# Kernel optimization log

Hardware: AMD Instinct MI355X
Metric: run time of the kernel (lower is better)

Reference implementation:

```python
import jax, jax.numpy as jnp
import numpy as np

N_NODES = 50000
N_EDGES = 800000
DIM = 128
N_GRAPHS = 512
LEVELS = [2, 2, 2]  # GCN layers per hierarchy level
N_LAYERS = sum(LEVELS)
EPS = 1e-5


def setup_inputs() -> dict:
    key = jax.random.key(0)
    ks = jax.random.split(key, 8)
    x = jax.random.normal(ks[0], (N_NODES, DIM), dtype=jnp.float32)
    edge_index = jax.random.randint(ks[1], (2, N_EDGES), 0, N_NODES, dtype=jnp.int64)
    batch = jnp.sort(jax.random.randint(ks[2], (N_NODES,), 0, N_GRAPHS, dtype=jnp.int64))
    # stacked per-layer GCN params (all layers are DIM->DIM since input_dim==hidden_dim)
    s = 1.0 / np.sqrt(DIM)
    W = jax.random.uniform(ks[3], (N_LAYERS, DIM, DIM), minval=-s, maxval=s, dtype=jnp.float32)
    b = jnp.zeros((N_LAYERS, DIM), dtype=jnp.float32)
    gamma = jnp.ones((N_LAYERS, DIM), dtype=jnp.float32)
    beta = jnp.zeros((N_LAYERS, DIM), dtype=jnp.float32)
    sf = 1.0 / np.sqrt(DIM * len(LEVELS))
    Wf = jax.random.uniform(ks[4], (DIM * len(LEVELS), DIM), minval=-sf, maxval=sf, dtype=jnp.float32)
    bf = jnp.zeros((DIM,), dtype=jnp.float32)
    return {"x": x, "edge_index": edge_index, "batch": batch,
            "W": W, "b": b, "gamma": gamma, "beta": beta, "Wf": Wf, "bf": bf}


def reference(x, edge_index, batch, W, b, gamma, beta, Wf, bf):
    N = x.shape[0]
    # GCNConv: add self-loops, symmetric normalization deg^-1/2 A_hat deg^-1/2
    loop = jnp.arange(N, dtype=edge_index.dtype)
    src = jnp.concatenate([edge_index[0], loop])
    dst = jnp.concatenate([edge_index[1], loop])
    deg = jax.ops.segment_sum(jnp.ones_like(dst, dtype=x.dtype), dst, num_segments=N)
    dinv = jnp.where(deg > 0, jax.lax.rsqrt(deg), 0.0)
    norm = dinv[src] * dinv[dst]  # (E+N,)

    def gcn(h, Wl, bl):
        h = h @ Wl                                   # (N, DIM)
        msg = h[src] * norm[:, None]                 # gather + scale, (E+N, DIM)
        return jax.ops.segment_sum(msg, dst, num_segments=N) + bl

    def batchnorm_relu(h, g, be):
        mu = jnp.mean(h, axis=0)
        var = jnp.mean(jnp.square(h - mu), axis=0)   # biased var (training-mode BN)
        return jax.nn.relu(g * (h - mu) * jax.lax.rsqrt(var + EPS) + be)

    counts = jax.ops.segment_sum(jnp.ones((N,), x.dtype), batch, num_segments=N_GRAPHS)
    counts = jnp.maximum(counts, 1.0)[:, None]

    reps = []
    h = x
    li = 0
    for num_layers in LEVELS:
        for _ in range(num_layers):
            h = batchnorm_relu(gcn(h, W[li], b[li]), gamma[li], beta[li])
            li += 1
        reps.append(jax.ops.segment_sum(h, batch, num_segments=N_GRAPHS) / counts)
    fused = jnp.concatenate(reps, axis=1)            # (G, 3*DIM)
    return jax.nn.relu(fused @ Wf + bf)              # dropout is identity at inference
```

## Files before the change

kernel.cpp:

```cpp
#include <hip/hip_runtime.h>
#include <hip/hip_fp16.h>


#define DIM 128
#define NGRAPH 512
#define EPSV 1e-5f


__global__ __launch_bounds__(256) void k_count(const int* __restrict__ ei, int* __restrict__ cnt, int E) {
  int e = blockIdx.x * 256 + threadIdx.x;
  if (e < E) atomicAdd(&cnt[ei[E + e]], 1);
}

__global__ __launch_bounds__(512) void k_blocksum(const int* __restrict__ cnt, int* __restrict__ partial, int N) {
  __shared__ int sd[512];
  int idx = blockIdx.x * 512 + threadIdx.x;
  int v = (idx < N) ? cnt[idx] : 0;
  sd[threadIdx.x] = v;
  __syncthreads();
  for (int ofs = 256; ofs > 0; ofs >>= 1) {
    if (threadIdx.x < ofs) sd[threadIdx.x] += sd[threadIdx.x + ofs];
    __syncthreads();
  }
  if (threadIdx.x == 0) partial[blockIdx.x] = sd[0];
}

__global__ __launch_bounds__(128) void k_scanpartials(int* __restrict__ partial, int nb) {
  __shared__ int sp[128];
  int t = threadIdx.x;
  int v = (t < nb) ? partial[t] : 0;
  sp[t] = v;
  __syncthreads();
  for (int ofs = 1; ofs < 128; ofs <<= 1) {
    int a = (t >= ofs) ? sp[t - ofs] : 0;
    __syncthreads();
    sp[t] += a;
    __syncthreads();
  }
  if (t < nb) partial[t] = sp[t] - v;
}

__global__ __launch_bounds__(512) void k_scan_write(const int* __restrict__ cnt, const int* __restrict__ partial,
                                                    int* __restrict__ rowptr, float* __restrict__ dinv, int N) {
  __shared__ int sd[512];
  int tid = threadIdx.x;
  int idx = blockIdx.x * 512 + tid;
  int v = (idx < N) ? cnt[idx] : 0;
  sd[tid] = v;
  __syncthreads();
  for (int ofs = 1; ofs < 512; ofs <<= 1) {
    int a = (tid >= ofs) ? sd[tid - ofs] : 0;
    __syncthreads();
    sd[tid] += a;
    __syncthreads();
  }
  if (idx < N) {
    int excl = partial[blockIdx.x] + sd[tid] - v;
    rowptr[idx] = excl;
    dinv[idx] = rsqrtf((float)(v + 1));
    if (idx == N - 1) rowptr[N] = excl + v;
  }
}

__global__ __launch_bounds__(256) void k_fill(const int* __restrict__ ei, const int* __restrict__ rowptr,
                                              int* __restrict__ cursor, unsigned short* __restrict__ cols, int E) {
  int e = blockIdx.x * 256 + threadIdx.x;
  if (e >= E) return;
  int s = ei[e];
  int d = ei[E + e];
  int pos = rowptr[d] + atomicAdd(&cursor[d], 1);
  cols[pos] = (unsigned short)s;
}

__global__ __launch_bounds__(256) void k_gstart(const int* __restrict__ batch, int* __restrict__ start, int N) {
  int i = blockIdx.x * 256 + threadIdx.x;
  if (i >= N) return;
  int bi = batch[i];
  int prev = (i == 0) ? -1 : batch[i - 1];
  for (int g = prev + 1; g <= bi; ++g) start[g] = i;
  if (i == N - 1) {
    for (int g = bi + 1; g <= NGRAPH; ++g) start[g] = N;
  }
}

__global__ __launch_bounds__(512) void k_invcnt(const int* __restrict__ start, float* __restrict__ invcnt) {
  int g = threadIdx.x;
  if (g < NGRAPH) {
    int c = start[g + 1] - start[g];
    invcnt[g] = 1.0f / (float)max(c, 1);
  }
}


__device__ inline void fma4(float4& ar, float a, const float4& wv) {
  ar.x = fmaf(a, wv.x, ar.x);
  ar.y = fmaf(a, wv.y, ar.y);
  ar.z = fmaf(a, wv.z, ar.z);
  ar.w = fmaf(a, wv.w, ar.w);
}

__global__ __launch_bounds__(256) void k_gemm(const float* __restrict__ A32,
                                              const unsigned int* __restrict__ A16,
                                              const float* __restrict__ Wl,
                                              const float* __restrict__ scsh,
                                              const float* __restrict__ dinv,
                                              unsigned int* __restrict__ T, float* __restrict__ stats, int N) {
  __shared__ float sH[64][DIM];
  int tid = threadIdx.x;
  size_t pstride = (size_t)(N + 1) * 16;
  if (blockIdx.x == 0) {
    stats[tid] = 0.f;
    if (tid < 64) {
      int p = tid >> 4, sl = tid & 15;
      T[(size_t)p * pstride + (size_t)N * 16 + sl] = 0u;
    }
  }
  int row0 = blockIdx.x * 64;
#pragma unroll
  for (int i = 0; i < 8; ++i) {
    int fi = tid + i * 256;
    int r = fi >> 5, c4 = fi & 31;
    int row = row0 + r;
    float4 v = make_float4(0.f, 0.f, 0.f, 0.f);
    if (scsh) {
      if (row < N) {
        uint2 u = ((const uint2*)(A16 + (size_t)row * 64))[c4];
        float2 lo = __half22float2(*(__half2*)&u.x);
        float2 hi = __half22float2(*(__half2*)&u.y);
        float4 sc = ((const float4*)scsh)[c4];
        float4 sh = ((const float4*)(scsh + DIM))[c4];
        v.x = fmaxf(fmaf(lo.x, sc.x, sh.x), 0.f);
        v.y = fmaxf(fmaf(lo.y, sc.y, sh.y), 0.f);
        v.z = fmaxf(fmaf(hi.x, sc.z, sh.z), 0.f);
        v.w = fmaxf(fmaf(hi.y, sc.w, sh.w), 0.f);
      }
    } else {
      if (row < N) v = ((const float4*)(A32 + (size_t)row * DIM))[c4];
    }
    ((float4*)&sH[r][0])[c4] = v;
  }
  __syncthreads();
  int ct = tid & 31, rt = tid >> 5;
  const float4* Wv = (const float4*)Wl;
  float4 acc[8];
#pragma unroll
  for (int r = 0; r < 8; ++r) acc[r] = make_float4(0.f, 0.f, 0.f, 0.f);
  for (int k4 = 0; k4 < 32; ++k4) {
    float4 wv0 = Wv[(4 * k4 + 0) * 32 + ct];
    float4 wv1 = Wv[(4 * k4 + 1) * 32 + ct];
    float4 wv2 = Wv[(4 * k4 + 2) * 32 + ct];
    float4 wv3 = Wv[(4 * k4 + 3) * 32 + ct];
#pragma unroll
    for (int r = 0; r < 8; ++r) {
      float4 av = *(const float4*)&sH[rt + 8 * r][4 * k4];
      fma4(acc[r], av.x, wv0);
      fma4(acc[r], av.y, wv1);
      fma4(acc[r], av.z, wv2);
      fma4(acc[r], av.w, wv3);
    }
  }
  int panel = ct >> 3;
  int psl = (ct & 7) * 2;
  unsigned int* Tp = T + (size_t)panel * pstride;
#pragma unroll
  for (int r = 0; r < 8; ++r) {
    int row = row0 + rt + 8 * r;
    if (row < N) {
      float dr = dinv[row];
      __half2 h0 = __floats2half2_rn(acc[r].x * dr, acc[r].y * dr);
      __half2 h1 = __floats2half2_rn(acc[r].z * dr, acc[r].w * dr);
      uint2 packed = make_uint2(*(unsigned int*)&h0, *(unsigned int*)&h1);
      *(uint2*)(Tp + (size_t)row * 16 + psl) = packed;
    }
  }
}

__global__ __launch_bounds__(256) void k_agg(const unsigned int* __restrict__ T, const int* __restrict__ rowptr,
                                             const unsigned short* __restrict__ cols, const float* __restrict__ dinv,
                                             const float* __restrict__ bias, unsigned int* __restrict__ hout,
                                             float* __restrict__ stats, int N) {
  int phase = blockIdx.x & 3;
  int chunk = blockIdx.x >> 2;
  int nchunks = gridDim.x >> 2;
  int tid = threadIdx.x;
  int wid = __builtin_amdgcn_readfirstlane(tid >> 6);
  int lane = tid & 63;
  int sub = lane >> 4;
  int slot = lane & 15;
  const unsigned int* __restrict__ Tp = T + (size_t)phase * (N + 1) * 16;
  float bx = bias[phase * 32 + 2 * slot];
  float by = bias[phase * 32 + 2 * slot + 1];
  int gwave = chunk * 4 + wid;
  int nwaves = nchunks * 4;
  float sum0 = 0.f, sum1 = 0.f, sq0 = 0.f, sq1 = 0.f;
  for (int i = gwave; i < N; i += nwaves) {
    float ax = 0.f, ay = 0.f;
    if (sub == 0) {
      unsigned int u0 = Tp[(size_t)i * 16 + slot];
      float2 t0 = __half22float2(*(__half2*)&u0);
      ax = t0.x;
      ay = t0.y;
    }
    int beg = rowptr[i], end = rowptr[i + 1];
    for (int e0 = beg; e0 < end; e0 += 32) {
      int ss[8];
#pragma unroll
      for (int k = 0; k < 8; ++k) {
        int eidx = e0 + 4 * k + sub;
        int cv = (int)cols[eidx];
        ss[k] = (eidx < end) ? cv : N;
      }
      unsigned int uu[8];
#pragma unroll
      for (int k = 0; k < 8; ++k) uu[k] = Tp[(size_t)ss[k] * 16 + slot];
#pragma unroll
      for (int k = 0; k < 8; ++k) {
        float2 t = __half22float2(*(__half2*)&uu[k]);
        ax += t.x;
        ay += t.y;
      }
    }
    ax += __shfl_xor(ax, 16);
    ay += __shfl_xor(ay, 16);
    ax += __shfl_xor(ax, 32);
    ay += __shfl_xor(ay, 32);
    if (sub == 0) {
      float di = dinv[i];
      ax = fmaf(di, ax, bx);
      ay = fmaf(di, ay, by);
      __half2 hp = __floats2half2_rn(ax, ay);
      hout[(size_t)i * 64 + phase * 16 + slot] = *(unsigned int*)&hp;
      sum0 += ax;
      sum1 += ay;
      sq0 = fmaf(ax, ax, sq0);
      sq1 = fmaf(ay, ay, sq1);
    }
  }
  __shared__ float red[4][16][4];
  if (sub == 0) {
    red[wid][slot][0] = sum0;
    red[wid][slot][1] = sum1;
    red[wid][slot][2] = sq0;
    red[wid][slot][3] = sq1;
  }
  __syncthreads();
  if (tid < 16) {
    int sl = tid;
    float a0 = red[0][sl][0] + red[1][sl][0] + red[2][sl][0] + red[3][sl][0];
    float a1 = red[0][sl][1] + red[1][sl][1] + red[2][sl][1] + red[3][sl][1];
    float q0 = red[0][sl][2] + red[1][sl][2] + red[2][sl][2] + red[3][sl][2];
    float q1 = red[0][sl][3] + red[1][sl][3] + red[2][sl][3] + red[3][sl][3];
    int c0 = phase * 32 + 2 * sl;
    atomicAdd(&stats[c0], a0);
    atomicAdd(&stats[c0 + 1], a1);
    atomicAdd(&stats[DIM + c0], q0);
    atomicAdd(&stats[DIM + c0 + 1], q1);
  }
}

__global__ __launch_bounds__(128) void k_bnstat(float* __restrict__ stats, const float* __restrict__ gamma,
                                                const float* __restrict__ beta, int N) {
  int c = threadIdx.x;
  float invN = 1.f / (float)N;
  float mu = stats[c] * invN;
  float var = stats[DIM + c] * invN - mu * mu;
  float rstd = rsqrtf(var + EPSV);
  float sc = gamma[c] * rstd;
  stats[2 * DIM + c] = sc;
  stats[3 * DIM + c] = beta[c] - mu * sc;
}

__global__ __launch_bounds__(512) void k_pool(const unsigned int* __restrict__ h16, const int* __restrict__ start,
                                              const float* __restrict__ invcnt, const float* __restrict__ scsh,
                                              float* __restrict__ pooled, int level) {
  int g = blockIdx.x;
  int s = start[g], e = start[g + 1];
  int slot = threadIdx.x & 63;
  int stripe = threadIdx.x >> 6;
  float scx = scsh[2 * slot], scy = scsh[2 * slot + 1];
  float shx = scsh[DIM + 2 * slot], shy = scsh[DIM + 2 * slot + 1];
  float ax = 0.f, ay = 0.f;
  for (int r = s + stripe; r < e; r += 8) {
    unsigned int u = h16[(size_t)r * 64 + slot];
    float2 t = __half22float2(*(__half2*)&u);
    ax += fmaxf(fmaf(t.x, scx, shx), 0.f);
    ay += fmaxf(fmaf(t.y, scy, shy), 0.f);
  }
  __shared__ float red[8][64][2];
  red[stripe][slot][0] = ax;
  red[stripe][slot][1] = ay;
  __syncthreads();
  if (threadIdx.x < 64) {
    int sl = threadIdx.x;
    float vx = 0.f, vy = 0.f;
#pragma unroll
    for (int st = 0; st < 8; ++st) {
      vx += red[st][sl][0];
      vy += red[st][sl][1];
    }
    float ic = invcnt[g];
    float* dst = pooled + (size_t)g * (3 * DIM) + level * DIM + 2 * sl;
    dst[0] = vx * ic;
    dst[1] = vy * ic;
  }
}

__global__ __launch_bounds__(512) void k_final(const float* __restrict__ pooled, const float* __restrict__ Wf,
                                               const float* __restrict__ bf, float* __restrict__ out) {
  int t = blockIdx.x * 512 + threadIdx.x;
  if (t >= NGRAPH * DIM) return;
  int j = t & (DIM - 1);
  int i = t >> 7;
  const float* prow = pooled + (size_t)i * (3 * DIM);
  float acc = bf[j];
  for (int k = 0; k < 3 * DIM; ++k) acc = fmaf(prow[k], Wf[(size_t)k * DIM + j], acc);
  out[t] = fmaxf(acc, 0.f);
}


extern "C" void kernel_launch(void* const* d_in, const int* in_sizes, int n_in,
                              void* d_out, int out_size, void* d_ws, size_t ws_size,
                              hipStream_t stream) {
  const float* x = (const float*)d_in[0];
  const int* ei = (const int*)d_in[1];
  const int* batch = (const int*)d_in[2];
  const float* W = (const float*)d_in[3];
  const float* b = (const float*)d_in[4];
  const float* gamma = (const float*)d_in[5];
  const float* beta = (const float*)d_in[6];
  const float* Wf = (const float*)d_in[7];
  const float* bf = (const float*)d_in[8];
  float* out = (float*)d_out;

  const int N = in_sizes[0] / DIM;
  const int E = in_sizes[1] / 2;

  char* base = (char*)d_ws;
  size_t off = 0;
  auto alloc = [&](size_t bytes) -> char* {
    char* p = base + off;
    off += (bytes + 255) & ~(size_t)255;
    return p;
  };
  unsigned int* h16 = (unsigned int*)alloc((size_t)N * DIM * 2);
  unsigned int* T   = (unsigned int*)alloc((size_t)(N + 1) * DIM * 2);
  int* cnt          = (int*)alloc((size_t)N * 4);
  int* cursor       = (int*)alloc((size_t)N * 4);
  int* rowptr       = (int*)alloc((size_t)(N + 1) * 4);
  int* partial      = (int*)alloc(256 * 4);
  float* dinv       = (float*)alloc((size_t)N * 4);
  unsigned short* cols = (unsigned short*)alloc((size_t)(E + 32) * 2);
  float* stats      = (float*)alloc(4 * DIM * 4);
  int* start        = (int*)alloc((NGRAPH + 1) * 4);
  float* invcnt     = (float*)alloc(NGRAPH * 4);
  float* pooled     = (float*)alloc((size_t)NGRAPH * 3 * DIM * 4);
  (void)ws_size;

  (void)hipMemsetAsync(cnt, 0, (size_t)N * 4, stream);
  (void)hipMemsetAsync(cursor, 0, (size_t)N * 4, stream);

  int nbScan = (N + 511) / 512;
  k_count<<<(E + 255) / 256, 256, 0, stream>>>(ei, cnt, E);
  k_blocksum<<<nbScan, 512, 0, stream>>>(cnt, partial, N);
  k_scanpartials<<<1, 128, 0, stream>>>(partial, nbScan);
  k_scan_write<<<nbScan, 512, 0, stream>>>(cnt, partial, rowptr, dinv, N);
  k_fill<<<(E + 255) / 256, 256, 0, stream>>>(ei, rowptr, cursor, cols, E);
  k_gstart<<<(N + 255) / 256, 256, 0, stream>>>(batch, start, N);
  k_invcnt<<<1, 512, 0, stream>>>(start, invcnt);

  int gemmGrid = (N + 63) / 64;
  for (int l = 0; l < 6; ++l) {
    const float* scsh = (l == 0) ? nullptr : stats + 2 * DIM;
    k_gemm<<<gemmGrid, 256, 0, stream>>>((l == 0) ? x : nullptr, (l == 0) ? nullptr : h16,
                                         W + (size_t)l * DIM * DIM, scsh, dinv, T, stats, N);
    k_agg<<<2048, 256, 0, stream>>>(T, rowptr, cols, dinv, b + (size_t)l * DIM, h16, stats, N);
    k_bnstat<<<1, 128, 0, stream>>>(stats, gamma + (size_t)l * DIM, beta + (size_t)l * DIM, N);
    if (l & 1) k_pool<<<NGRAPH, 512, 0, stream>>>(h16, start, invcnt, stats + 2 * DIM, pooled, l >> 1);
  }
  k_final<<<(NGRAPH * DIM + 511) / 512, 512, 0, stream>>>(pooled, Wf, bf, out);
}
```

Baseline: 779.4 us.

## Use fp16 MFMA for per-layer GEMM and fold BN stat finalize into consumers

Replaces the scalar FP32 FMA GEMM with fp16 MFMA 16x16x32 instructions, using a pre-transposed fp16 copy of the weights made once per call and staged in LDS with padded pitch. The output tile is repacked through LDS for coalesced panel stores. The separate BN statistics finalize kernel is removed: each layer gets its own zero-initialized stats buffer, and scale/shift are computed inside the next GEMM and the pooling kernel. Inputs to the matmul are now rounded to fp16, which loses some precision on the first layer's fp32 input.

```diff
diff --git a/kernel.cpp b/kernel.cpp
--- a/kernel.cpp
+++ b/kernel.cpp
@@ -5,6 +5,9 @@
 #define DIM 128
 #define NGRAPH 512
 #define EPSV 1e-5f
+
+typedef _Float16 f16x8 __attribute__((ext_vector_type(8)));
+typedef float f32x4 __attribute__((ext_vector_type(4)));
 
 
 __global__ __launch_bounds__(256) void k_count(const int* __restrict__ ei, int* __restrict__ cnt, int E) {
@@ -91,86 +94,115 @@
   }
 }
 
-
-__device__ inline void fma4(float4& ar, float a, const float4& wv) {
-  ar.x = fmaf(a, wv.x, ar.x);
-  ar.y = fmaf(a, wv.y, ar.y);
-  ar.z = fmaf(a, wv.z, ar.z);
-  ar.w = fmaf(a, wv.w, ar.w);
-}
+__global__ __launch_bounds__(256) void k_prepw(const float* __restrict__ W, _Float16* __restrict__ W16T) {
+  int idx = blockIdx.x * 256 + threadIdx.x;
+  if (idx >= 6 * 16384) return;
+  int l = idx >> 14, rem = idx & 16383;
+  int k = rem >> 7, n = rem & 127;
+  W16T[(size_t)l * 16384 + (size_t)n * 128 + k] = (_Float16)W[(size_t)l * 16384 + (size_t)k * 128 + n];
+}
+
+
+#define PITCH 136
 
 __global__ __launch_bounds__(256) void k_gemm(const float* __restrict__ A32,
                                               const unsigned int* __restrict__ A16,
-                                              const float* __restrict__ Wl,
-                                              const float* __restrict__ scsh,
+                                              const _Float16* __restrict__ W16T,
+                                              const float* __restrict__ statsPrev,
+                                              const float* __restrict__ gammaP, const float* __restrict__ betaP,
                                               const float* __restrict__ dinv,
-                                              unsigned int* __restrict__ T, float* __restrict__ stats, int N) {
-  __shared__ float sH[64][DIM];
+                                              unsigned int* __restrict__ T, int N) {
+  __shared__ _Float16 sW[128 * PITCH];
+  __shared__ _Float16 sA[64 * PITCH];
+  __shared__ float sScSh[256];
   int tid = threadIdx.x;
   size_t pstride = (size_t)(N + 1) * 16;
-  if (blockIdx.x == 0) {
-    stats[tid] = 0.f;
-    if (tid < 64) {
-      int p = tid >> 4, sl = tid & 15;
-      T[(size_t)p * pstride + (size_t)N * 16 + sl] = 0u;
-    }
-  }
+  if (blockIdx.x == 0 && tid < 64) {
+    int p = tid >> 4, sl = tid & 15;
+    T[(size_t)p * pstride + (size_t)N * 16 + sl] = 0u;
+  }
+  if (statsPrev && tid < 128) {
+    float invN = 1.f / (float)N;
+    float mu = statsPrev[tid] * invN;
+    float var = statsPrev[128 + tid] * invN - mu * mu;
+    float sc = gammaP[tid] * rsqrtf(var + EPSV);
+    sScSh[tid] = sc;
+    sScSh[128 + tid] = betaP[tid] - mu * sc;
+  }
+#pragma unroll
+  for (int i = 0; i < 16; ++i) {
+    int f = (tid + i * 256) * 4;
+    int n = f >> 7, k = f & 127;
+    *(uint2*)&sW[n * PITCH + k] = *(const uint2*)&W16T[n * 128 + k];
+  }
+  __syncthreads();
   int row0 = blockIdx.x * 64;
 #pragma unroll
   for (int i = 0; i < 8; ++i) {
-    int fi = tid + i * 256;
-    int r = fi >> 5, c4 = fi & 31;
+    int f = (tid + i * 256) * 4;
+    int r = f >> 7, c = f & 127;
     int row = row0 + r;
-    float4 v = make_float4(0.f, 0.f, 0.f, 0.f);
-    if (scsh) {
-      if (row < N) {
-        uint2 u = ((const uint2*)(A16 + (size_t)row * 64))[c4];
+    uint2 outp = make_uint2(0u, 0u);
+    if (row < N) {
+      float v0, v1, v2, v3;
+      if (statsPrev) {
+        uint2 u = *(const uint2*)&A16[(size_t)row * 64 + (c >> 1)];
         float2 lo = __half22float2(*(__half2*)&u.x);
         float2 hi = __half22float2(*(__half2*)&u.y);
-        float4 sc = ((const float4*)scsh)[c4];
-        float4 sh = ((const float4*)(scsh + DIM))[c4];
-        v.x = fmaxf(fmaf(lo.x, sc.x, sh.x), 0.f);
-        v.y = fmaxf(fmaf(lo.y, sc.y, sh.y), 0.f);
-        v.z = fmaxf(fmaf(hi.x, sc.z, sh.z), 0.f);
-        v.w = fmaxf(fmaf(hi.y, sc.w, sh.w), 0.f);
+        v0 = fmaxf(fmaf(lo.x, sScSh[c], sScSh[128 + c]), 0.f);
+        v1 = fmaxf(fmaf(lo.y, sScSh[c + 1], sScSh[128 + c + 1]), 0.f);
+        v2 = fmaxf(fmaf(hi.x, sScSh[c + 2], sScSh[128 + c + 2]), 0.f);
+        v3 = fmaxf(fmaf(hi.y, sScSh[c + 3], sScSh[128 + c + 3]), 0.f);
+      } else {
+        float4 v = *(const float4*)&A32[(size_t)row * 128 + c];
+        v0 = v.x; v1 = v.y; v2 = v.z; v3 = v.w;
       }
-    } else {
-      if (row < N) v = ((const float4*)(A32 + (size_t)row * DIM))[c4];
-    }
-    ((float4*)&sH[r][0])[c4] = v;
-  }
-  __syncthreads();
-  int ct = tid & 31, rt = tid >> 5;
-  const float4* Wv = (const float4*)Wl;
-  float4 acc[8];
-#pragma unroll
-  for (int r = 0; r < 8; ++r) acc[r] = make_float4(0.f, 0.f, 0.f, 0.f);
-  for (int k4 = 0; k4 < 32; ++k4) {
-    float4 wv0 = Wv[(4 * k4 + 0) * 32 + ct];
-    float4 wv1 = Wv[(4 * k4 + 1) * 32 + ct];
-    float4 wv2 = Wv[(4 * k4 + 2) * 32 + ct];
-    float4 wv3 = Wv[(4 * k4 + 3) * 32 + ct];
-#pragma unroll
-    for (int r = 0; r < 8; ++r) {
-      float4 av = *(const float4*)&sH[rt + 8 * r][4 * k4];
-      fma4(acc[r], av.x, wv0);
-      fma4(acc[r], av.y, wv1);
-      fma4(acc[r], av.z, wv2);
-      fma4(acc[r], av.w, wv3);
-    }
-  }
-  int panel = ct >> 3;
-  int psl = (ct & 7) * 2;
-  unsigned int* Tp = T + (size_t)panel * pstride;
-#pragma unroll
-  for (int r = 0; r < 8; ++r) {
-    int row = row0 + rt + 8 * r;
+      __half2 h0 = __floats2half2_rn(v0, v1);
+      __half2 h1 = __floats2half2_rn(v2, v3);
+      outp = make_uint2(*(unsigned int*)&h0, *(unsigned int*)&h1);
+    }
+    *(uint2*)&sA[r * PITCH + c] = outp;
+  }
+  __syncthreads();
+  int w = tid >> 6;
+  int l = tid & 63;
+  int m = l & 15, kg = l >> 4;
+  int rowbase = 16 * w;
+  f16x8 af[4];
+#pragma unroll
+  for (int ks = 0; ks < 4; ++ks)
+    af[ks] = *(const f16x8*)&sA[(rowbase + m) * PITCH + ks * 32 + kg * 8];
+  f32x4 acc[8] = {};
+#pragma unroll
+  for (int t8 = 0; t8 < 8; ++t8) {
+#pragma unroll
+    for (int ks = 0; ks < 4; ++ks) {
+      f16x8 bf = *(const f16x8*)&sW[(t8 * 16 + m) * PITCH + ks * 32 + kg * 8];
+      acc[t8] = __builtin_amdgcn_mfma_f32_16x16x32_f16(af[ks], bf, acc[t8], 0, 0, 0);
+    }
+  }
+  float dv[4];
+#pragma unroll
+  for (int j = 0; j < 4; ++j) {
+    int row = row0 + rowbase + kg * 4 + j;
+    dv[j] = (row < N) ? dinv[row] : 0.f;
+  }
+#pragma unroll
+  for (int t8 = 0; t8 < 8; ++t8) {
+#pragma unroll
+    for (int j = 0; j < 4; ++j)
+      sA[(rowbase + kg * 4 + j) * PITCH + t8 * 16 + m] = (_Float16)(acc[t8][j] * dv[j]);
+  }
+  __syncthreads();
+#pragma unroll
+  for (int i = 0; i < 8; ++i) {
+    int idx = tid + i * 256;
+    int r = idx >> 5, q = idx & 31;
+    int row = row0 + r;
     if (row < N) {
-      float dr = dinv[row];
-      __half2 h0 = __floats2half2_rn(acc[r].x * dr, acc[r].y * dr);
-      __half2 h1 = __floats2half2_rn(acc[r].z * dr, acc[r].w * dr);
-      uint2 packed = make_uint2(*(unsigned int*)&h0, *(unsigned int*)&h1);
-      *(uint2*)(Tp + (size_t)row * 16 + psl) = packed;
+      uint2 val = *(const uint2*)((const char*)sA + r * (PITCH * 2) + q * 8);
+      int p = q >> 3, psl = (q & 7) * 2;
+      *(uint2*)&T[(size_t)p * pstride + (size_t)row * 16 + psl] = val;
     }
   }
 }
@@ -258,27 +290,23 @@
   }
 }
 
-__global__ __launch_bounds__(128) void k_bnstat(float* __restrict__ stats, const float* __restrict__ gamma,
-                                                const float* __restrict__ beta, int N) {
-  int c = threadIdx.x;
-  float invN = 1.f / (float)N;
-  float mu = stats[c] * invN;
-  float var = stats[DIM + c] * invN - mu * mu;
-  float rstd = rsqrtf(var + EPSV);
-  float sc = gamma[c] * rstd;
-  stats[2 * DIM + c] = sc;
-  stats[3 * DIM + c] = beta[c] - mu * sc;
-}
-
 __global__ __launch_bounds__(512) void k_pool(const unsigned int* __restrict__ h16, const int* __restrict__ start,
-                                              const float* __restrict__ invcnt, const float* __restrict__ scsh,
-                                              float* __restrict__ pooled, int level) {
+                                              const float* __restrict__ invcnt, const float* __restrict__ statsL,
+                                              const float* __restrict__ gammaL, const float* __restrict__ betaL,
+                                              float* __restrict__ pooled, int level, int N) {
   int g = blockIdx.x;
   int s = start[g], e = start[g + 1];
   int slot = threadIdx.x & 63;
   int stripe = threadIdx.x >> 6;
-  float scx = scsh[2 * slot], scy = scsh[2 * slot + 1];
-  float shx = scsh[DIM + 2 * slot], shy = scsh[DIM + 2 * slot + 1];
+  float invN = 1.f / (float)N;
+  int c0 = 2 * slot, c1 = c0 + 1;
+  float mu0 = statsL[c0] * invN, mu1 = statsL[c1] * invN;
+  float var0 = statsL[DIM + c0] * invN - mu0 * mu0;
+  float var1 = statsL[DIM + c1] * invN - mu1 * mu1;
+  float scx = gammaL[c0] * rsqrtf(var0 + EPSV);
+  float scy = gammaL[c1] * rsqrtf(var1 + EPSV);
+  float shx = betaL[c0] - mu0 * scx;
+  float shy = betaL[c1] - mu1 * scy;
   float ax = 0.f, ay = 0.f;
   for (int r = s + stripe; r < e; r += 8) {
     unsigned int u = h16[(size_t)r * 64 + slot];
@@ -344,13 +372,14 @@
   };
   unsigned int* h16 = (unsigned int*)alloc((size_t)N * DIM * 2);
   unsigned int* T   = (unsigned int*)alloc((size_t)(N + 1) * DIM * 2);
+  _Float16* W16T    = (_Float16*)alloc((size_t)6 * 16384 * 2);
   int* cnt          = (int*)alloc((size_t)N * 4);
   int* cursor       = (int*)alloc((size_t)N * 4);
   int* rowptr       = (int*)alloc((size_t)(N + 1) * 4);
   int* partial      = (int*)alloc(256 * 4);
   float* dinv       = (float*)alloc((size_t)N * 4);
   unsigned short* cols = (unsigned short*)alloc((size_t)(E + 32) * 2);
-  float* stats      = (float*)alloc(4 * DIM * 4);
+  float* statsAll   = (float*)alloc(6 * 256 * 4);
   int* start        = (int*)alloc((NGRAPH + 1) * 4);
   float* invcnt     = (float*)alloc(NGRAPH * 4);
   float* pooled     = (float*)alloc((size_t)NGRAPH * 3 * DIM * 4);
@@ -358,6 +387,7 @@
 
   (void)hipMemsetAsync(cnt, 0, (size_t)N * 4, stream);
   (void)hipMemsetAsync(cursor, 0, (size_t)N * 4, stream);
+  (void)hipMemsetAsync(statsAll, 0, 6 * 256 * 4, stream);
 
   int nbScan = (N + 511) / 512;
   k_count<<<(E + 255) / 256, 256, 0, stream>>>(ei, cnt, E);
@@ -367,15 +397,21 @@
   k_fill<<<(E + 255) / 256, 256, 0, stream>>>(ei, rowptr, cursor, cols, E);
   k_gstart<<<(N + 255) / 256, 256, 0, stream>>>(batch, start, N);
   k_invcnt<<<1, 512, 0, stream>>>(start, invcnt);
+  k_prepw<<<(6 * 16384 + 255) / 256, 256, 0, stream>>>(W, W16T);
 
   int gemmGrid = (N + 63) / 64;
   for (int l = 0; l < 6; ++l) {
-    const float* scsh = (l == 0) ? nullptr : stats + 2 * DIM;
+    const float* statsPrev = (l == 0) ? nullptr : statsAll + (l - 1) * 256;
+    const float* gP = (l == 0) ? gamma : gamma + (size_t)(l - 1) * DIM;
+    const float* bP = (l == 0) ? beta : beta + (size_t)(l - 1) * DIM;
     k_gemm<<<gemmGrid, 256, 0, stream>>>((l == 0) ? x : nullptr, (l == 0) ? nullptr : h16,
-                                         W + (size_t)l * DIM * DIM, scsh, dinv, T, stats, N);
-    k_agg<<<2048, 256, 0, stream>>>(T, rowptr, cols, dinv, b + (size_t)l * DIM, h16, stats, N);
-    k_bnstat<<<1, 128, 0, stream>>>(stats, gamma + (size_t)l * DIM, beta + (size_t)l * DIM, N);
-    if (l & 1) k_pool<<<NGRAPH, 512, 0, stream>>>(h16, start, invcnt, stats + 2 * DIM, pooled, l >> 1);
+                                         W16T + (size_t)l * 16384, statsPrev, gP, bP, dinv, T, N);
+    k_agg<<<2048, 256, 0, stream>>>(T, rowptr, cols, dinv, b + (size_t)l * DIM, h16,
+                                    statsAll + (size_t)l * 256, N);
+    if (l & 1)
+      k_pool<<<NGRAPH, 512, 0, stream>>>(h16, start, invcnt, statsAll + (size_t)l * 256,
+                                         gamma + (size_t)l * DIM, beta + (size_t)l * DIM,
+                                         pooled, l >> 1, N);
   }
   k_final<<<(NGRAPH * DIM + 511) / 512, 512, 0, stream>>>(pooled, Wf, bf, out);
 }
```

Measured after the change: 693.6 us. -11.0%, faster.
